# Optimization experiments

Hardware: AMD Instinct MI355X
Metric: run time of the kernel (lower is better)

Reference implementation:

```python
import jax, jax.numpy as jnp
import numpy as np

EMBED = 1024
HEADS = 16
HEAD_DIM = EMBED // HEADS


def setup_inputs() -> dict:
    key = jax.random.key(0)
    ks = jax.random.split(key, 10)
    B, S = 2, 2048
    x = jax.random.normal(ks[0], (B, S, EMBED), dtype=jnp.float32)
    s = 1.0 / np.sqrt(EMBED)
    Wq = jax.random.normal(ks[1], (EMBED, EMBED), dtype=jnp.float32) * s
    Wk = jax.random.normal(ks[2], (EMBED, EMBED), dtype=jnp.float32) * s
    Wv = jax.random.normal(ks[3], (EMBED, EMBED), dtype=jnp.float32) * s
    Wo = jax.random.normal(ks[4], (EMBED, EMBED), dtype=jnp.float32) * s
    bq = jnp.zeros((EMBED,), jnp.float32)
    bk = jnp.zeros((EMBED,), jnp.float32)
    bv = jnp.zeros((EMBED,), jnp.float32)
    bo = jnp.zeros((EMBED,), jnp.float32)
    J = jax.random.normal(ks[5], (HEADS, HEAD_DIM, HEAD_DIM), dtype=jnp.float32) * 0.02
    lam = jnp.asarray(0.5, jnp.float32)
    return {"x": x, "Wq": Wq, "bq": bq, "Wk": Wk, "bk": bk,
            "Wv": Wv, "bv": bv, "Wo": Wo, "bo": bo, "J": J, "lam": lam}


def reference(x, Wq, bq, Wk, bk, Wv, bv, Wo, bo, J, lam):
    B, S, E = x.shape
    H, hd = HEADS, HEAD_DIM
    scale = np.sqrt(hd).astype(np.float32)

    def split_heads(t):  # (B,S,E) -> (B,H,S,hd)
        return t.reshape(B, S, H, hd).transpose(0, 2, 1, 3)

    Q = split_heads(x @ Wq + bq)
    K = split_heads(x @ Wk + bk)
    V = split_heads(x @ Wv + bv)

    scores = jnp.einsum('bhid,bhjd->bhij', Q, K) / scale
    Qn = jnp.tanh(Q)
    Kn = jnp.tanh(K)
    # bilinear correction: tanh(Q) J tanh(K)^T per head
    delta = jnp.einsum('bhid,hde,bhje->bhij', Qn, J, Kn)
    scores = scores + lam * delta

    causal = jnp.triu(jnp.ones((S, S), dtype=bool), k=1)  # True above diagonal
    scores = jnp.where(causal[None, None], -jnp.inf, scores)

    probs = jax.nn.softmax(scores, axis=-1)
    out = jnp.einsum('bhij,bhjd->bhid', probs, V)
    out = out.transpose(0, 2, 1, 3).reshape(B, S, E)
    return out @ Wo + bo
```

## Files before the change

### kernel.cpp

```cpp
#include <hip/hip_runtime.h>
#include <cstdint>
#include <cstddef>

typedef __bf16 bf16x8 __attribute__((ext_vector_type(8)));
typedef short  s16x8  __attribute__((ext_vector_type(8)));
typedef float  f32x4  __attribute__((ext_vector_type(4)));
typedef unsigned int u32x4 __attribute__((ext_vector_type(4)));
typedef unsigned int u32x2 __attribute__((ext_vector_type(2)));

#define MFMA16(a, b, c) __builtin_amdgcn_mfma_f32_16x16x32_bf16((a), (b), (c), 0, 0, 0)

typedef __attribute__((address_space(3))) unsigned int       lds_uint;
typedef const __attribute__((address_space(1))) unsigned int glb_uint;

static __device__ __forceinline__ void gload_lds16(const void* g, void* l) {
  __builtin_amdgcn_global_load_lds((glb_uint*)g, (lds_uint*)l, 16, 0, 0);
}

static __device__ __forceinline__ unsigned short f2bf(float f) {
  unsigned u = __builtin_bit_cast(unsigned, f);
  unsigned r = u + 0x7FFFu + ((u >> 16) & 1u);
  return (unsigned short)(r >> 16);
}
static __device__ __forceinline__ float bf2f(unsigned short u) {
  unsigned x = ((unsigned)u) << 16;
  return __builtin_bit_cast(float, x);
}
static __device__ __forceinline__ float fast_tanh(float x) {
  float e = __expf(2.f * x);
  return 1.f - 2.f / (e + 1.f);
}
static __device__ __forceinline__ unsigned cvt_pk_bf16(float lo, float hi) {
  unsigned r;
  asm("v_cvt_pk_bf16_f32 %0, %1, %2" : "=v"(r) : "v"(lo), "v"(hi));
  return r;
}
static __device__ __forceinline__ float exp2_(float x) {
  float r;
  asm("v_exp_f32 %0, %1\n\ts_nop 0" : "=v"(r) : "v"(x));
  return r;
}
static __device__ __forceinline__ u32x4 tanh8(u32x4 q, float mul) {
  u32x4 o;
#pragma unroll
  for (int j = 0; j < 4; ++j) {
    float lo = bf2f((unsigned short)(q[j] & 0xffffu)) * mul;
    float hi = bf2f((unsigned short)(q[j] >> 16)) * mul;
    o[j] = cvt_pk_bf16(fast_tanh(lo), fast_tanh(hi));
  }
  return o;
}

__global__ void k_f32_to_bf16(const float* __restrict__ src,
                              unsigned short* __restrict__ dst, int n4) {
  int i = blockIdx.x * blockDim.x + threadIdx.x;
  if (i >= n4) return;
  float4 v = reinterpret_cast<const float4*>(src)[i];
  ushort4 o;
  o.x = f2bf(v.x); o.y = f2bf(v.y); o.z = f2bf(v.z); o.w = f2bf(v.w);
  reinterpret_cast<ushort4*>(dst)[i] = o;
}

__global__ void k_transpose4_to_bf16(const float* __restrict__ s0,
                                     const float* __restrict__ s1,
                                     const float* __restrict__ s2,
                                     const float* __restrict__ s3,
                                     unsigned short* __restrict__ dstBase) {
  __shared__ float t[32][33];
  const int z = blockIdx.z;
  const float* src = (z == 0) ? s0 : (z == 1) ? s1 : (z == 2) ? s2 : s3;
  unsigned short* dst = dstBase + (size_t)z * 1048576;
  int c0 = blockIdx.x * 32, r0 = blockIdx.y * 32;
  int tx = threadIdx.x, ty = threadIdx.y;
#pragma unroll
  for (int i = 0; i < 4; ++i)
    t[ty + i * 8][tx] = src[(size_t)(r0 + ty + i * 8) * 1024 + c0 + tx];
  __syncthreads();
#pragma unroll
  for (int i = 0; i < 4; ++i)
    dst[(size_t)(c0 + ty + i * 8) * 1024 + r0 + tx] = f2bf(t[tx][ty + i * 8]);
}

__global__ __launch_bounds__(256) void k_gemm_op(
    const unsigned short* __restrict__ A, const unsigned short* __restrict__ Bt,
    int M, int N, int K,
    float* __restrict__ Cout, const float* __restrict__ bias) {
  __shared__ __align__(16) unsigned short Al[2][128 * 64];
  __shared__ __align__(16) unsigned short Bl[2][128 * 64];
  const int tid = threadIdx.x;
  const int lane = tid & 63, w = tid >> 6;
  const int wm = w >> 1, wn = w & 1;
  const int l15 = lane & 15, l4 = lane >> 4;
  const int m0 = blockIdx.y * 128, n0 = blockIdx.x * 128;
  const int NT = K >> 6;

  const int srow = lane >> 3;
  const int schunk = (lane & 7) ^ srow;
  const unsigned short* Ag = A + (size_t)(m0 + (w << 5) + srow) * K + (schunk << 3);
  const unsigned short* Bg = Bt + (size_t)(n0 + (w << 5) + srow) * K + (schunk << 3);

  auto stage = [&](int slot, int t) {
    unsigned short* Alw = &Al[slot][0] + (w << 5) * 64;
    unsigned short* Blw = &Bl[slot][0] + (w << 5) * 64;
#pragma unroll
    for (int p = 0; p < 4; ++p) {
      gload_lds16(Ag + (size_t)(p * 8) * K + t * 64, Alw + p * 8 * 64);
      gload_lds16(Bg + (size_t)(p * 8) * K + t * 64, Blw + p * 8 * 64);
    }
  };

  const f32x4 zero4 = {0.f, 0.f, 0.f, 0.f};
  f32x4 acc[4][4];
#pragma unroll
  for (int i = 0; i < 4; ++i)
#pragma unroll
    for (int j = 0; j < 4; ++j) acc[i][j] = zero4;

  stage(0, 0);
  __syncthreads();

  for (int t = 0; t < NT; ++t) {
    const int s = t & 1;
    const int tn = (t + 1 < NT) ? t + 1 : NT - 1;
    stage(s ^ 1, tn);
    const char* As = (const char*)&Al[s][0];
    const char* Bs = (const char*)&Bl[s][0];
#pragma unroll
    for (int c = 0; c < 2; ++c) {
      bf16x8 af[4], bfr[4];
#pragma unroll
      for (int i = 0; i < 4; ++i) {
        int ra = wm * 64 + i * 16 + l15;
        af[i] = *reinterpret_cast<const bf16x8*>(
            As + ra * 128 + ((c * 64 + l4 * 16) ^ ((ra & 7) << 4)));
        int rb = wn * 64 + i * 16 + l15;
        bfr[i] = *reinterpret_cast<const bf16x8*>(
            Bs + rb * 128 + ((c * 64 + l4 * 16) ^ ((rb & 7) << 4)));
      }
      __builtin_amdgcn_s_setprio(1);
#pragma unroll
      for (int i = 0; i < 4; ++i)
#pragma unroll
        for (int j = 0; j < 4; ++j) acc[i][j] = MFMA16(af[i], bfr[j], acc[i][j]);
      __builtin_amdgcn_s_setprio(0);
    }
    __syncthreads();
  }

#pragma unroll
  for (int i = 0; i < 4; ++i)
#pragma unroll
    for (int j = 0; j < 4; ++j)
#pragma unroll
      for (int r = 0; r < 4; ++r) {
        int mrow = m0 + wm * 64 + i * 16 + l4 * 4 + r;
        int ncol = n0 + wn * 64 + j * 16 + l15;
        Cout[(size_t)mrow * N + ncol] = acc[i][j][r] + bias[ncol];
      }
}

__global__ __launch_bounds__(512, 2) void k_gemm256_qkv(
    const unsigned short* __restrict__ A, const unsigned short* __restrict__ Bt,
    int M, int N, int K,
    const float* __restrict__ bq, const float* __restrict__ bk,
    const float* __restrict__ bv,
    unsigned short* __restrict__ Qa, unsigned short* __restrict__ Ka,
    unsigned short* __restrict__ Vt, unsigned short* __restrict__ Qn) {
  __shared__ __align__(16) unsigned short SLDS[4 * 256 * 64];
  const int tid = threadIdx.x;
  const int lane = tid & 63;
  const int w = tid >> 6, wm = w >> 2, wn = w & 3;
  const int l15 = lane & 15, l4 = lane >> 4;
  const int nbx = N >> 8;
  const int bid = (int)blockIdx.x;
  const int lin = (bid & 7) * ((int)gridDim.x >> 3) + (bid >> 3);
  const int m0 = (lin / nbx) << 8, n0 = (lin % nbx) << 8;
  const int NT = K >> 6;

  const int strow = tid >> 3, stchunk = tid & 7;
  const int schunk = stchunk ^ (strow & 7);

  auto stage = [&](int slot, int kt) {
    unsigned short* Ad = SLDS + slot * 16384;
    unsigned short* Bd = SLDS + (2 + slot) * 16384;
#pragma unroll
    for (int i = 0; i < 4; ++i) {
      int row = i * 64 + strow;
      gload_lds16(A + (size_t)(m0 + row) * K + kt * 64 + schunk * 8,
                  Ad + row * 64 + stchunk * 8);
      gload_lds16(Bt + (size_t)(n0 + row) * K + kt * 64 + schunk * 8,
                  Bd + row * 64 + stchunk * 8);
    }
  };

  const f32x4 zero4 = {0.f, 0.f, 0.f, 0.f};
  f32x4 acc[8][4];
#pragma unroll
  for (int i = 0; i < 8; ++i)
#pragma unroll
    for (int j = 0; j < 4; ++j) acc[i][j] = zero4;

  stage(0, 0);
  __syncthreads();

  bf16x8 af[4][2], bf0[2][2], bf1[2][2];

  for (int kt = 0; kt < NT; ++kt) {
    const int s = kt & 1;
    const char* As = (const char*)(SLDS + s * 16384);
    const char* Bs = (const char*)(SLDS + (2 + s) * 16384);
    const int kp1 = (kt + 1 < NT) ? kt + 1 : NT - 1;

    stage(s ^ 1, kp1);

#pragma unroll
    for (int i = 0; i < 4; ++i) {
      const int ra = wm * 128 + i * 16 + l15;
#pragma unroll
      for (int kk = 0; kk < 2; ++kk)
        af[i][kk] = *(const bf16x8*)(As + ra * 128 + (((kk * 4 + l4) ^ (ra & 7)) << 4));
    }
#pragma unroll
    for (int j = 0; j < 2; ++j) {
      const int rb = wn * 64 + j * 16 + l15;
#pragma unroll
      for (int kk = 0; kk < 2; ++kk)
        bf0[j][kk] = *(const bf16x8*)(Bs + rb * 128 + (((kk * 4 + l4) ^ (rb & 7)) << 4));
    }
    __builtin_amdgcn_s_setprio(1);
#pragma unroll
    for (int i = 0; i < 4; ++i)
#pragma unroll
      for (int j = 0; j < 2; ++j)
#pragma unroll
        for (int kk = 0; kk < 2; ++kk)
          acc[i][j] = MFMA16(af[i][kk], bf0[j][kk], acc[i][j]);
    __builtin_amdgcn_s_setprio(0);

#pragma unroll
    for (int j = 0; j < 2; ++j) {
      const int rb = wn * 64 + (2 + j) * 16 + l15;
#pragma unroll
      for (int kk = 0; kk < 2; ++kk)
        bf1[j][kk] = *(const bf16x8*)(Bs + rb * 128 + (((kk * 4 + l4) ^ (rb & 7)) << 4));
    }
    __builtin_amdgcn_s_setprio(1);
#pragma unroll
    for (int i = 0; i < 4; ++i)
#pragma unroll
      for (int j = 0; j < 2; ++j)
#pragma unroll
        for (int kk = 0; kk < 2; ++kk)
          acc[i][2 + j] = MFMA16(af[i][kk], bf1[j][kk], acc[i][2 + j]);
    __builtin_amdgcn_s_setprio(0);

#pragma unroll
    for (int i = 0; i < 4; ++i) {
      const int ra = wm * 128 + (4 + i) * 16 + l15;
#pragma unroll
      for (int kk = 0; kk < 2; ++kk)
        af[i][kk] = *(const bf16x8*)(As + ra * 128 + (((kk * 4 + l4) ^ (ra & 7)) << 4));
    }
    __builtin_amdgcn_s_setprio(1);
#pragma unroll
    for (int i = 0; i < 4; ++i)
#pragma unroll
      for (int j = 0; j < 2; ++j)
#pragma unroll
        for (int kk = 0; kk < 2; ++kk)
          acc[4 + i][2 + j] = MFMA16(af[i][kk], bf1[j][kk], acc[4 + i][2 + j]);

#pragma unroll
    for (int i = 0; i < 4; ++i)
#pragma unroll
      for (int j = 0; j < 2; ++j)
#pragma unroll
        for (int kk = 0; kk < 2; ++kk)
          acc[4 + i][j] = MFMA16(af[i][kk], bf0[j][kk], acc[4 + i][j]);
    __builtin_amdgcn_s_setprio(0);

    __syncthreads();
  }

  char* wbuf = reinterpret_cast<char*>(SLDS) + w * 16384;
  const int proj = n0 >> 10;
  const int nn0 = (n0 + wn * 64) & 1023;
  const int hh = nn0 >> 6;
  const int mbase = m0 + wm * 128;
  const int bb = mbase >> 11;
  const float* bias = (proj == 0) ? bq : (proj == 1) ? bk : bv;
  float bcol[4];
#pragma unroll
  for (int nf = 0; nf < 4; ++nf) bcol[nf] = bias[nn0 + nf * 16 + l15];

  if (proj == 2) {
#pragma unroll
    for (int mf = 0; mf < 8; ++mf) {
#pragma unroll
      for (int nf = 0; nf < 4; ++nf) {
        const int d = nf * 16 + l15;
        const int tok = mf * 16 + l4 * 4;
        u32x2 pk;
        pk[0] = cvt_pk_bf16(acc[mf][nf][0] + bcol[nf], acc[mf][nf][1] + bcol[nf]);
        pk[1] = cvt_pk_bf16(acc[mf][nf][2] + bcol[nf], acc[mf][nf][3] + bcol[nf]);
        *reinterpret_cast<u32x2*>(
            wbuf + d * 256 + (((tok >> 3) ^ (d & 7)) << 4) + (tok & 7) * 2) = pk;
      }
    }
    __syncthreads();
    const size_t vbase = (size_t)(bb * 16 + hh) * 64 * 2048;
#pragma unroll
    for (int dblk = 0; dblk < 8; ++dblk) {
#pragma unroll
      for (int thalf = 0; thalf < 2; ++thalf) {
        const int d = (lane >> 3) + dblk * 8;
        const int tch = (lane & 7) + thalf * 8;
        u32x4 vv = *reinterpret_cast<const u32x4*>(
            wbuf + d * 256 + ((tch ^ (d & 7)) << 4));
        const int sidx = (mbase + tch * 8) & 2047;
        *reinterpret_cast<u32x4*>(Vt + vbase + (size_t)d * 2048 + sidx) = vv;
      }
    }
  } else {
#pragma unroll
    for (int mf = 0; mf < 8; ++mf) {
#pragma unroll
      for (int nf = 0; nf < 4; ++nf) {
        const int d = nf * 16 + l15;
#pragma unroll
        for (int r = 0; r < 4; ++r) {
          float v = acc[mf][nf][r] + bcol[nf];
          if (proj == 0) v *= 0.18033688f;
          const int tok = mf * 16 + l4 * 4 + r;
          *reinterpret_cast<unsigned short*>(wbuf + tok * 128 + d * 2) = f2bf(v);
        }
      }
    }
    __syncthreads();
    const size_t t64base = (size_t)(bb * 16 + hh) * 2048;
#pragma unroll
    for (int iter = 0; iter < 16; ++iter) {
      const int tl = (lane >> 3) + iter * 8;
      const int dc = lane & 7;
      u32x4 q8 = *reinterpret_cast<const u32x4*>(wbuf + tl * 128 + dc * 16);
      const size_t t64 = t64base + ((mbase + tl) & 2047);
      if (proj == 0) {
        *reinterpret_cast<u32x4*>(Qa + t64 * 128 + dc * 8) = q8;
        u32x4 qn = tanh8(q8, 5.54517744f);
        *reinterpret_cast<u32x4*>(Qn + t64 * 64 + dc * 8) = qn;
      } else {
        *reinterpret_cast<u32x4*>(Ka + t64 * 128 + dc * 8) = q8;
        u32x4 kn = tanh8(q8, 1.0f);
        *reinterpret_cast<u32x4*>(Ka + t64 * 128 + 64 + dc * 8) = kn;
      }
    }
  }
}

__global__ __launch_bounds__(256) void k_qnj(const unsigned short* __restrict__ Qn,
                                             const float* __restrict__ J,
                                             const float* __restrict__ lamPtr,
                                             unsigned short* __restrict__ Qa) {
  __shared__ float Jl[64 * 64];
  __shared__ float Ql[64 * 64];
  int bid = blockIdx.x;
  int bh = bid >> 5, sblk = bid & 31;
  int h = bh & 15;
  int tid = threadIdx.x;
  float lam = lamPtr[0] * 1.44269504f;
  const float4* Jh = reinterpret_cast<const float4*>(J + (size_t)h * 4096);
#pragma unroll
  for (int p = 0; p < 4; ++p)
    reinterpret_cast<float4*>(Jl)[p * 256 + tid] = Jh[p * 256 + tid];
  size_t tok0 = (size_t)bh * 2048 + sblk * 64;
#pragma unroll
  for (int p = 0; p < 2; ++p) {
    int idx = p * 256 + tid;
    s16x8 v = *reinterpret_cast<const s16x8*>(Qn + tok0 * 64 + idx * 8);
#pragma unroll
    for (int j = 0; j < 8; ++j) Ql[idx * 8 + j] = bf2f((unsigned short)v[j]);
  }
  __syncthreads();
  int e = tid & 63, wq = tid >> 6;
#pragma unroll 1
  for (int pass = 0; pass < 16; ++pass) {
    int tok = pass * 4 + wq;
    float a0 = 0.f, a1 = 0.f;
#pragma unroll
    for (int d = 0; d < 64; d += 2) {
      a0 += Ql[tok * 64 + d] * Jl[d * 64 + e];
      a1 += Ql[tok * 64 + d + 1] * Jl[(d + 1) * 64 + e];
    }
    Qa[(tok0 + tok) * 128 + 64 + e] = f2bf(lam * (a0 + a1));
  }
}

__global__ __launch_bounds__(256) void k_attn(const unsigned short* __restrict__ Qa,
                                              const unsigned short* __restrict__ Ka,
                                              const unsigned short* __restrict__ Vt,
                                              unsigned short* __restrict__ Ob) {
  constexpr int S = 2048;
  __shared__ __align__(16) unsigned short Klds[2][64 * 128];
  __shared__ __align__(16) unsigned short Vtl[2][64 * 64];

  const int blk = (int)blockIdx.x;
  const int xg = blk & 7, idx = blk >> 3;
  const int bh = xg * 4 + (idx & 3);
  const int qt = 31 - (idx >> 2);
  const int b = bh >> 4, h = bh & 15;
  const int tid = threadIdx.x;
  const int lane = tid & 63, w = tid >> 6;
  const int l15 = lane & 15, l4 = lane >> 4;
  const int q0 = qt * 64;
  const size_t bhS = (size_t)bh * S;
  const unsigned short* Kbase = Ka + bhS * 128;
  const unsigned short* Vbase = Vt + (size_t)bh * 64 * 2048;
  const f32x4 zero4 = {0.f, 0.f, 0.f, 0.f};

  const int rowbase = w * 16 + (lane >> 4);
  const int rb7 = rowbase & 7;
  const int cK0 = (lane & 15) ^ rb7;
  const int cK1 = cK0 ^ 4;
  const int vdvrow = w * 16 + (lane >> 3);
  const int cV = (lane & 7) ^ ((lane >> 3) & 7);

  bf16x8 qf[4];
  {
    int qrow = q0 + w * 16 + l15;
#pragma unroll
    for (int c = 0; c < 4; ++c)
      qf[c] = *reinterpret_cast<const bf16x8*>(Qa + (bhS + qrow) * 128 + c * 32 + l4 * 8);
  }

  f32x4 oacc[4];
  float m_ = -__builtin_inff(), lsum = 0.f;
#pragma unroll
  for (int v = 0; v < 4; ++v) oacc[v] = zero4;

  const int I0 = (l15 + 32 * (l4 & 1)) * 4;
  const int I1 = I0 + 64;
  const bool hi4 = (lane & 32) != 0;

#pragma unroll
  for (int p = 0; p < 4; ++p)
    gload_lds16(Kbase + (size_t)(rowbase + 4 * p) * 128 + ((p & 1) ? cK1 : cK0) * 8,
                &Klds[0][(w * 16 + p * 4) * 128]);
#pragma unroll
  for (int p = 0; p < 2; ++p)
    gload_lds16(Vbase + (size_t)(vdvrow + 8 * p) * 2048 + cV * 8,
                &Vtl[0][(w * 16 + p * 8) * 64]);
  __syncthreads();

  for (int kt = 0; kt <= qt; ++kt) {
    const int cur = kt & 1;
    const bool lastStep = (kt == qt);

    if (!lastStep) {
      const int base = (kt + 1) * 64;
      const int nxt = cur ^ 1;
#pragma unroll
      for (int p = 0; p < 4; ++p)
        gload_lds16(Kbase + (size_t)(base + rowbase + 4 * p) * 128 + ((p & 1) ? cK1 : cK0) * 8,
                    &Klds[nxt][(w * 16 + p * 4) * 128]);
#pragma unroll
      for (int p = 0; p < 2; ++p)
        gload_lds16(Vbase + (size_t)(vdvrow + 8 * p) * 2048 + base + cV * 8,
                    &Vtl[nxt][(w * 16 + p * 8) * 64]);
    }

    const char* Kl = reinterpret_cast<const char*>(Klds[cur]);
    f32x4 sc[4];
    __builtin_amdgcn_s_setprio(1);
#pragma unroll
    for (int fn = 0; fn < 4; ++fn) {
      sc[fn] = zero4;
      const int krow = fn * 16 + l15;
#pragma unroll
      for (int c = 0; c < 4; ++c) {
        bf16x8 kf = *reinterpret_cast<const bf16x8*>(
            Kl + krow * 256 + (((c * 4 + l4) ^ (krow & 7)) << 4));
        sc[fn] = MFMA16(kf, qf[c], sc[fn]);
      }
    }
    __builtin_amdgcn_s_setprio(0);

    if (lastStep) {
      const int qloc = w * 16 + l15;
#pragma unroll
      for (int fn = 0; fn < 4; ++fn)
#pragma unroll
        for (int r = 0; r < 4; ++r)
          if (fn * 16 + l4 * 4 + r > qloc) sc[fn][r] = -__builtin_inff();
    }

    float mx = sc[0][0];
#pragma unroll
    for (int fn = 0; fn < 4; ++fn)
#pragma unroll
      for (int r = 0; r < 4; ++r) mx = fmaxf(mx, sc[fn][r]);
    mx = fmaxf(mx, __shfl_xor(mx, 16));
    mx = fmaxf(mx, __shfl_xor(mx, 32));
    if (!__all(mx - m_ <= 11.5f)) {
      const float mn = fmaxf(m_, mx);
      const float al = exp2_(m_ - mn);
      lsum *= al;
      m_ = mn;
#pragma unroll
      for (int r = 0; r < 4; ++r) {
        float albc = __shfl(al, l4 * 4 + r);
#pragma unroll
        for (int v = 0; v < 4; ++v) oacc[v][r] *= albc;
      }
    }
    float p_[4][4];
    float rs = 0.f;
#pragma unroll
    for (int fn = 0; fn < 4; ++fn)
#pragma unroll
      for (int r = 0; r < 4; ++r) {
        float e = exp2_(sc[fn][r] - m_);
        p_[fn][r] = e;
        rs += e;
      }
    rs += __shfl_xor(rs, 16);
    rs += __shfl_xor(rs, 32);
    lsum += rs;

    unsigned cp[4][2];
#pragma unroll
    for (int fn = 0; fn < 4; ++fn) {
      cp[fn][0] = cvt_pk_bf16(p_[fn][0], p_[fn][1]);
      cp[fn][1] = cvt_pk_bf16(p_[fn][2], p_[fn][3]);
    }

    const char* Vl = reinterpret_cast<const char*>(Vtl[cur]);
#pragma unroll
    for (int c2 = 0; c2 < 2; ++c2) {
      unsigned a0 = __builtin_amdgcn_ds_bpermute(I0, (int)cp[c2 * 2][0]);
      unsigned b0 = __builtin_amdgcn_ds_bpermute(I0, (int)cp[c2 * 2 + 1][0]);
      unsigned a1 = __builtin_amdgcn_ds_bpermute(I0, (int)cp[c2 * 2][1]);
      unsigned b1 = __builtin_amdgcn_ds_bpermute(I0, (int)cp[c2 * 2 + 1][1]);
      unsigned a2 = __builtin_amdgcn_ds_bpermute(I1, (int)cp[c2 * 2][0]);
      unsigned b2 = __builtin_amdgcn_ds_bpermute(I1, (int)cp[c2 * 2 + 1][0]);
      unsigned a3 = __builtin_amdgcn_ds_bpermute(I1, (int)cp[c2 * 2][1]);
      unsigned b3 = __builtin_amdgcn_ds_bpermute(I1, (int)cp[c2 * 2 + 1][1]);
      u32x4 pw = {hi4 ? b0 : a0, hi4 ? b1 : a1, hi4 ? b2 : a2, hi4 ? b3 : a3};
      bf16x8 pa = __builtin_bit_cast(bf16x8, pw);
      __builtin_amdgcn_s_setprio(1);
#pragma unroll
      for (int v = 0; v < 4; ++v) {
        const int dvrow = v * 16 + l15;
        bf16x8 vf = *reinterpret_cast<const bf16x8*>(
            Vl + dvrow * 128 + (((c2 * 4 + l4) ^ (dvrow & 7)) << 4));
        oacc[v] = MFMA16(pa, vf, oacc[v]);
      }
      __builtin_amdgcn_s_setprio(0);
    }

    __syncthreads();
  }

  float lbc[4];
#pragma unroll
  for (int r = 0; r < 4; ++r) lbc[r] = __shfl(lsum, l4 * 4 + r);
#pragma unroll
  for (int v = 0; v < 4; ++v) {
#pragma unroll
    for (int r = 0; r < 4; ++r) {
      int row = q0 + w * 16 + l4 * 4 + r;
      float o = oacc[v][r] / lbc[r];
      Ob[((size_t)b * S + row) * 1024 + h * 64 + v * 16 + l15] = f2bf(o);
    }
  }
}

extern "C" void kernel_launch(void* const* d_in, const int* in_sizes, int n_in,
                              void* d_out, int out_size, void* d_ws, size_t ws_size,
                              hipStream_t stream) {
  const float* x   = (const float*)d_in[0];
  const float* Wq  = (const float*)d_in[1];
  const float* bq  = (const float*)d_in[2];
  const float* Wk  = (const float*)d_in[3];
  const float* bk  = (const float*)d_in[4];
  const float* Wv  = (const float*)d_in[5];
  const float* bv  = (const float*)d_in[6];
  const float* Wo  = (const float*)d_in[7];
  const float* bo  = (const float*)d_in[8];
  const float* J   = (const float*)d_in[9];
  const float* lam = (const float*)d_in[10];
  float* out = (float*)d_out;

  char* ws = (char*)d_ws;
  unsigned short* xb     = (unsigned short*)(ws);
  unsigned short* Wt_qkv = (unsigned short*)(ws + 8388608);
  unsigned short* Wt_o   = (unsigned short*)(ws + 14680064);
  unsigned short* Qa     = (unsigned short*)(ws + 16777216);
  unsigned short* Ka     = (unsigned short*)(ws + 33554432);
  unsigned short* Vt     = (unsigned short*)(ws + 50331648);
  unsigned short* Qn     = (unsigned short*)(ws + 58720256);
  unsigned short* Ob     = (unsigned short*)(ws + 67108864);

  k_f32_to_bf16<<<4096, 256, 0, stream>>>(x, xb, 1048576);

  k_transpose4_to_bf16<<<dim3(32, 32, 4), dim3(32, 8), 0, stream>>>(
      Wq, Wk, Wv, Wo, Wt_qkv);

  k_gemm256_qkv<<<192, 512, 0, stream>>>(xb, Wt_qkv, 4096, 3072, 1024,
      bq, bk, bv, Qa, Ka, Vt, Qn);

  k_qnj<<<1024, 256, 0, stream>>>(Qn, J, lam, Qa);

  k_attn<<<1024, 256, 0, stream>>>(Qa, Ka, Vt, Ob);

  k_gemm_op<<<dim3(8, 32), 256, 0, stream>>>(Ob, Wt_o, 4096, 1024, 1024,
      out, bo);
}
```

Baseline: 158.5 us.

## Drop LDS staging in attention kernel and read K/V directly from global

Removes the double-buffered LDS staging of K and V tiles and the per-tile block barrier. Each wave now loads its MFMA operands for K and V straight from global memory, relying on the caches. The query-tile order over blocks is also reshuffled to interleave long and short causal rows, and the exp and bf16 pack steps are merged into one loop. The cost is that all four waves fetch the same K/V tile redundantly, and there is no explicit prefetch to hide global load latency behind the MFMAs.

```diff
diff --git a/kernel.cpp b/kernel.cpp
--- a/kernel.cpp
+++ b/kernel.cpp
@@ -400,33 +400,29 @@
                                               const unsigned short* __restrict__ Vt,
                                               unsigned short* __restrict__ Ob) {
   constexpr int S = 2048;
-  __shared__ __align__(16) unsigned short Klds[2][64 * 128];
-  __shared__ __align__(16) unsigned short Vtl[2][64 * 64];
-
   const int blk = (int)blockIdx.x;
-  const int xg = blk & 7, idx = blk >> 3;
-  const int bh = xg * 4 + (idx & 3);
-  const int qt = 31 - (idx >> 2);
+  const int xg = blk & 7;
+  const int rest = blk >> 3;
+  const int bhsel = rest & 3;
+  const int g = rest >> 2;
+  const int jq = g >> 3, iq = g & 7;
+  const int qgroup = (jq == 0) ? (31 - iq) : (jq == 1) ? (16 + iq)
+                   : (jq == 2) ? (15 - iq) : iq;
+  const int bh = xg * 4 + bhsel;
   const int b = bh >> 4, h = bh & 15;
   const int tid = threadIdx.x;
   const int lane = tid & 63, w = tid >> 6;
   const int l15 = lane & 15, l4 = lane >> 4;
-  const int q0 = qt * 64;
+  const int q0 = qgroup * 64 + w * 16;
+  const int NT = qgroup + 1;
   const size_t bhS = (size_t)bh * S;
   const unsigned short* Kbase = Ka + bhS * 128;
   const unsigned short* Vbase = Vt + (size_t)bh * 64 * 2048;
   const f32x4 zero4 = {0.f, 0.f, 0.f, 0.f};
 
-  const int rowbase = w * 16 + (lane >> 4);
-  const int rb7 = rowbase & 7;
-  const int cK0 = (lane & 15) ^ rb7;
-  const int cK1 = cK0 ^ 4;
-  const int vdvrow = w * 16 + (lane >> 3);
-  const int cV = (lane & 7) ^ ((lane >> 3) & 7);
-
   bf16x8 qf[4];
   {
-    int qrow = q0 + w * 16 + l15;
+    int qrow = q0 + l15;
 #pragma unroll
     for (int c = 0; c < 4; ++c)
       qf[c] = *reinterpret_cast<const bf16x8*>(Qa + (bhS + qrow) * 128 + c * 32 + l4 * 8);
@@ -441,56 +437,29 @@
   const int I1 = I0 + 64;
   const bool hi4 = (lane & 32) != 0;
 
-#pragma unroll
-  for (int p = 0; p < 4; ++p)
-    gload_lds16(Kbase + (size_t)(rowbase + 4 * p) * 128 + ((p & 1) ? cK1 : cK0) * 8,
-                &Klds[0][(w * 16 + p * 4) * 128]);
-#pragma unroll
-  for (int p = 0; p < 2; ++p)
-    gload_lds16(Vbase + (size_t)(vdvrow + 8 * p) * 2048 + cV * 8,
-                &Vtl[0][(w * 16 + p * 8) * 64]);
-  __syncthreads();
-
-  for (int kt = 0; kt <= qt; ++kt) {
-    const int cur = kt & 1;
-    const bool lastStep = (kt == qt);
-
-    if (!lastStep) {
-      const int base = (kt + 1) * 64;
-      const int nxt = cur ^ 1;
-#pragma unroll
-      for (int p = 0; p < 4; ++p)
-        gload_lds16(Kbase + (size_t)(base + rowbase + 4 * p) * 128 + ((p & 1) ? cK1 : cK0) * 8,
-                    &Klds[nxt][(w * 16 + p * 4) * 128]);
-#pragma unroll
-      for (int p = 0; p < 2; ++p)
-        gload_lds16(Vbase + (size_t)(vdvrow + 8 * p) * 2048 + base + cV * 8,
-                    &Vtl[nxt][(w * 16 + p * 8) * 64]);
-    }
-
-    const char* Kl = reinterpret_cast<const char*>(Klds[cur]);
+  for (int kt = 0; kt < NT; ++kt) {
     f32x4 sc[4];
     __builtin_amdgcn_s_setprio(1);
 #pragma unroll
     for (int fn = 0; fn < 4; ++fn) {
       sc[fn] = zero4;
-      const int krow = fn * 16 + l15;
+      const size_t krow = (size_t)(kt * 64 + fn * 16 + l15);
 #pragma unroll
       for (int c = 0; c < 4; ++c) {
         bf16x8 kf = *reinterpret_cast<const bf16x8*>(
-            Kl + krow * 256 + (((c * 4 + l4) ^ (krow & 7)) << 4));
+            Kbase + krow * 128 + c * 32 + l4 * 8);
         sc[fn] = MFMA16(kf, qf[c], sc[fn]);
       }
     }
     __builtin_amdgcn_s_setprio(0);
 
-    if (lastStep) {
-      const int qloc = w * 16 + l15;
+    if (kt * 64 + 63 > q0) {
+      const int qloc = q0 + l15;
 #pragma unroll
       for (int fn = 0; fn < 4; ++fn)
 #pragma unroll
         for (int r = 0; r < 4; ++r)
-          if (fn * 16 + l4 * 4 + r > qloc) sc[fn][r] = -__builtin_inff();
+          if (kt * 64 + fn * 16 + l4 * 4 + r > qloc) sc[fn][r] = -__builtin_inff();
     }
 
     float mx = sc[0][0];
@@ -512,28 +481,22 @@
         for (int v = 0; v < 4; ++v) oacc[v][r] *= albc;
       }
     }
-    float p_[4][4];
     float rs = 0.f;
-#pragma unroll
-    for (int fn = 0; fn < 4; ++fn)
-#pragma unroll
-      for (int r = 0; r < 4; ++r) {
-        float e = exp2_(sc[fn][r] - m_);
-        p_[fn][r] = e;
-        rs += e;
-      }
+    unsigned cp[4][2];
+#pragma unroll
+    for (int fn = 0; fn < 4; ++fn) {
+      float e0 = exp2_(sc[fn][0] - m_);
+      float e1 = exp2_(sc[fn][1] - m_);
+      float e2 = exp2_(sc[fn][2] - m_);
+      float e3 = exp2_(sc[fn][3] - m_);
+      rs += (e0 + e1) + (e2 + e3);
+      cp[fn][0] = cvt_pk_bf16(e0, e1);
+      cp[fn][1] = cvt_pk_bf16(e2, e3);
+    }
     rs += __shfl_xor(rs, 16);
     rs += __shfl_xor(rs, 32);
     lsum += rs;
 
-    unsigned cp[4][2];
-#pragma unroll
-    for (int fn = 0; fn < 4; ++fn) {
-      cp[fn][0] = cvt_pk_bf16(p_[fn][0], p_[fn][1]);
-      cp[fn][1] = cvt_pk_bf16(p_[fn][2], p_[fn][3]);
-    }
-
-    const char* Vl = reinterpret_cast<const char*>(Vtl[cur]);
 #pragma unroll
     for (int c2 = 0; c2 < 2; ++c2) {
       unsigned a0 = __builtin_amdgcn_ds_bpermute(I0, (int)cp[c2 * 2][0]);
@@ -549,15 +512,13 @@
       __builtin_amdgcn_s_setprio(1);
 #pragma unroll
       for (int v = 0; v < 4; ++v) {
-        const int dvrow = v * 16 + l15;
+        const size_t dvrow = (size_t)(v * 16 + l15);
         bf16x8 vf = *reinterpret_cast<const bf16x8*>(
-            Vl + dvrow * 128 + (((c2 * 4 + l4) ^ (dvrow & 7)) << 4));
+            Vbase + dvrow * 2048 + kt * 64 + c2 * 32 + l4 * 8);
         oacc[v] = MFMA16(pa, vf, oacc[v]);
       }
       __builtin_amdgcn_s_setprio(0);
     }
-
-    __syncthreads();
   }
 
   float lbc[4];
@@ -567,7 +528,7 @@
   for (int v = 0; v < 4; ++v) {
 #pragma unroll
     for (int r = 0; r < 4; ++r) {
-      int row = q0 + w * 16 + l4 * 4 + r;
+      int row = q0 + l4 * 4 + r;
       float o = oacc[v][r] / lbc[r];
       Ob[((size_t)b * S + row) * 1024 + h * 64 + v * 16 + l15] = f2bf(o);
     }
```

After: 296.8 us (median of 2 runs). 87.3% more time.
